# Optimization experiments

Hardware: AMD Instinct MI355X
Metric: run time of the kernel (lower is better)

## Reference

```python
import jax, jax.numpy as jnp
import numpy as np

N_NODES = 100000
N_EDGES = 1600000
HIDDEN_DIM = 64
EIGS_DIM = 32


def setup_inputs() -> dict:
    key = jax.random.key(0)
    k1, k2, k3, k4, k5 = jax.random.split(key, 5)
    q = jax.random.normal(k1, (N_NODES, HIDDEN_DIM), dtype=jnp.float32)
    k = jax.random.normal(k2, (N_NODES, HIDDEN_DIM), dtype=jnp.float32)
    v = jax.random.normal(k3, (N_NODES, HIDDEN_DIM), dtype=jnp.float32)
    eigs = jax.random.normal(k4, (N_NODES, EIGS_DIM), dtype=jnp.float32)
    lambda0 = jnp.zeros((1,), dtype=jnp.float32)  # nn.Parameter(torch.zeros(1))
    indices = jax.random.randint(k5, (2, N_EDGES), 0, N_NODES, dtype=jnp.int64)
    return {"q": q, "k": k, "v": v, "eigs": eigs, "lambda0": lambda0,
            "indices": indices}


def reference(q, k, v, eigs, lambda0, indices):
    n = q.shape[0]
    inv_sqrt_dim = 1.0 / jnp.sqrt(jnp.asarray(q.shape[1], dtype=q.dtype))
    i0 = indices[0]  # destination/row node per edge
    i1 = indices[1]  # source/col node per edge

    # per-edge attention logits: gather-dot-product
    x = jnp.sum(q[i0] * k[i1], axis=-1) * inv_sqrt_dim          # [E]
    y = jnp.sum(eigs[i0] * eigs[i1], axis=-1)                   # [E]
    s = x + jnp.exp(lambda0[0]) * y                             # [E]

    # sparse softmax: clamp(exp(s), -5, 5) then segment-normalize by row sum
    e = jnp.clip(jnp.exp(s), -5.0, 5.0)                         # [E]
    denom = jax.ops.segment_sum(e, i0, num_segments=n)          # [N]
    denom = jnp.where(denom == 0.0, 1.0, denom)
    w = e / denom[i0]                                           # [E]

    # spmm: out[r] = sum_{edges with row r} w_e * v[col_e]
    out = jax.ops.segment_sum(w[:, None] * v[i1], i0, num_segments=n)  # [N, D]
    return out
```

## Files before the change

kernel.cpp:

```cpp
#include <hip/hip_runtime.h>
#include <hip/hip_fp16.h>


#define HD 64
#define ED 32
#define CAP 64
#define RPP 256
#define PSHIFT 8
#define D1 15
#define SLICE 16
#define SPILL_CAP 65536

struct h4 { __half2 a, b; };

__global__ void p1_bin_kernel(const int* __restrict__ idx, int n_edges,
                              int NP, int chunk, int nb, long long pcap,
                              int* __restrict__ part,
                              long long* __restrict__ spill,
                              int* __restrict__ spill_cnt,
                              int* __restrict__ flag,
                              const float* __restrict__ kf,
                              const float* __restrict__ vf,
                              const float* __restrict__ ef,
                              __half* __restrict__ k16,
                              __half* __restrict__ v16,
                              __half* __restrict__ e16,
                              long long nk4, long long ne4) {
    extern __shared__ int sm[];
    int* cnt  = sm;
    int* bins = sm + NP;
    int tid = threadIdx.x;

    for (int i = tid; i < NP; i += 256) cnt[i] = 0;
    __syncthreads();

    int e0 = blockIdx.x * chunk;
    int n  = n_edges - e0; if (n > chunk) n = chunk; if (n < 0) n = 0;

    for (int i = tid; i < n; i += 256) {
        int e = e0 + i;
        int r = idx[e];
        int c = idx[n_edges + e];
        int p = r >> PSHIFT;
        int w = ((r & (RPP - 1)) << 17) | c;
        int pos = atomicAdd(&cnt[p], 1);
        if (pos < D1) {
            bins[p * D1 + pos] = w;
        } else {
            int s = atomicAdd(spill_cnt, 1);
            if (s < SPILL_CAP) spill[s] = ((long long)r << 32) | (unsigned)c;
            else *flag = 1;
        }
    }
    __syncthreads();

    int g16 = tid >> 4;
    int sl  = tid & 15;
    for (int p = g16; p < NP; p += 16) {
        int m = cnt[p]; if (m > D1) m = D1;
        long long base = (long long)p * pcap + (long long)blockIdx.x * SLICE;
        int val = (sl == 0) ? m
                : (sl <= m) ? bins[p * D1 + sl - 1] : 0;
        part[base + sl] = val;
    }

    if (k16 != nullptr) {
        long long gt = (long long)blockIdx.x * 256 + tid;
        long long gs = (long long)gridDim.x * 256;
        for (long long t = gt; t < nk4; t += gs) {
            float4 f = ((const float4*)kf)[t];
            h4 h;
            h.a = __floats2half2_rn(f.x, f.y);
            h.b = __floats2half2_rn(f.z, f.w);
            ((h4*)k16)[t] = h;
        }
        for (long long t = gt; t < nk4; t += gs) {
            float4 f = ((const float4*)vf)[t];
            h4 h;
            h.a = __floats2half2_rn(f.x, f.y);
            h.b = __floats2half2_rn(f.z, f.w);
            ((h4*)v16)[t] = h;
        }
        for (long long t = gt; t < ne4; t += gs) {
            float4 f = ((const float4*)ef)[t];
            h4 h;
            h.a = __floats2half2_rn(f.x, f.y);
            h.b = __floats2half2_rn(f.z, f.w);
            ((h4*)e16)[t] = h;
        }
    }
}

__global__ void p2_bucket_kernel(const int* __restrict__ part,
                                 int* __restrict__ count,
                                 int* __restrict__ bucket, int n_nodes,
                                 int nb, long long pcap) {
    __shared__ int cnt2[RPP / 2];
    __shared__ int win[(RPP / 2) * CAP];
    int tid = threadIdx.x;
    if (tid < RPP / 2) cnt2[tid] = 0;
    __syncthreads();

    int p    = blockIdx.x >> 1;
    int half = blockIdx.x & 1;
    int g  = tid >> 4;
    int sl = tid & 15;
    const int* prow = part + (long long)p * pcap;

    for (int b = g; b < nb; b += 16) {
        int val = prow[b * SLICE + sl];
        int m = __shfl(val, 0, 16);
        if (m > D1) m = D1;
        if (sl >= 1 && sl <= m) {
            int rl = val >> 17;
            if ((rl >> 7) == half) {
                int rh = rl & 127;
                int c  = val & 0x1FFFF;
                int pos = atomicAdd(&cnt2[rh], 1);
                if (pos < CAP) win[(rh << 6) + pos] = c;
            }
        }
    }
    __syncthreads();

    int r0 = (p << PSHIFT) + (half << 7);
    int rows = n_nodes - r0;
    if (rows > RPP / 2) rows = RPP / 2;
    if (rows > 0) {
        int nint4 = rows * (CAP / 4);
        int4* dst = (int4*)(bucket + (long long)r0 * CAP);
        const int4* src = (const int4*)win;
        for (int i = tid; i < nint4; i += 256) dst[i] = src[i];
        if (tid < rows) count[r0 + tid] = cnt2[tid];
    }
}

__global__ void spill_or_zero_kernel(const long long* __restrict__ spill,
                                     const int* __restrict__ spill_cnt,
                                     const int* __restrict__ flag,
                                     int* __restrict__ count,
                                     int* __restrict__ bucket, int n_nodes) {
    int stride = gridDim.x * blockDim.x;
    int t0 = blockIdx.x * blockDim.x + threadIdx.x;
    if (*flag) {
        for (int t = t0; t < n_nodes; t += stride) count[t] = 0;
        return;
    }
    int ns = *spill_cnt; if (ns > SPILL_CAP) ns = SPILL_CAP;
    for (int t = t0; t < ns; t += stride) {
        long long wc = spill[t];
        int r = (int)(wc >> 32);
        int c = (int)(wc & 0xFFFFFFFFLL);
        int pos = atomicAdd(&count[r], 1);
        if (pos < CAP) bucket[(long long)r * CAP + pos] = c;
    }
}

__global__ void repair_scatter_kernel(const int* __restrict__ flag,
                                      const int* __restrict__ idx,
                                      int* __restrict__ count,
                                      int* __restrict__ bucket, int n_edges) {
    if (*flag == 0) return;
    int t = blockIdx.x * blockDim.x + threadIdx.x;
    if (t < n_edges) {
        int r = idx[t];
        int c = idx[n_edges + t];
        int p = atomicAdd(&count[r], 1);
        if (p < CAP) bucket[(long long)r * CAP + p] = c;
    }
}

__global__ void bucket_scatter_kernel(const int* __restrict__ idx,
                                      int* __restrict__ count,
                                      int* __restrict__ bucket, int n_edges) {
    int t = blockIdx.x * blockDim.x + threadIdx.x;
    if (t < n_edges) {
        int r = idx[t];
        int c = idx[n_edges + t];
        int p = atomicAdd(&count[r], 1);
        if (p < CAP) bucket[(long long)r * CAP + p] = c;
    }
}

__global__ void row16_kernel(const float* __restrict__ q,
                             const __half* __restrict__ k16,
                             const __half* __restrict__ v16,
                             const float* __restrict__ eigs,
                             const __half* __restrict__ e16,
                             const float* __restrict__ lambda0,
                             const int* __restrict__ counts,
                             const int* __restrict__ col,
                             const float* __restrict__ kf,
                             const float* __restrict__ vf,
                             const int* __restrict__ idx, int n_edges,
                             float* __restrict__ out, int n_nodes) {
    long long tid = (long long)blockIdx.x * blockDim.x + threadIdx.x;
    int r = (int)(tid >> 6);
    if (r >= n_nodes) return;
    int lane = threadIdx.x & 63;
    int sub = lane & 15;
    int grp = lane >> 4;

    int deg = counts[r];
    const float expL = __expf(lambda0[0]);

    if (deg > CAP) {
        float qs = q[(long long)r * HD + lane] * 0.125f;
        float gs = (lane < ED) ? eigs[(long long)r * ED + lane] * expL : 0.f;
        float accs = 0.f, den = 0.f;
        for (int base = 0; base < n_edges; base += 64) {
            int e = base + lane;
            int rr = (e < n_edges) ? idx[e] : -1;
            int cc = (e < n_edges) ? idx[n_edges + e] : 0;
            unsigned long long mm = __ballot(rr == r);
            while (mm) {
                int b = __ffsll(mm) - 1;
                mm &= mm - 1;
                int c = __shfl(cc, b, 64);
                float kb = kf[(long long)c * HD + lane];
                float gb = (lane < ED) ? eigs[(long long)c * ED + lane] : 0.f;
                float s = qs * kb + gs * gb;
                #pragma unroll
                for (int off = 32; off > 0; off >>= 1) s += __shfl_xor(s, off, 64);
                float e1 = fminf(__expf(s), 5.0f);
                den += e1;
                accs += e1 * vf[(long long)c * HD + lane];
            }
        }
        float inv = (den == 0.f) ? 1.f : __frcp_rn(den);
        out[(long long)r * HD + lane] = accs * inv;
        return;
    }

    long long start = (long long)r * CAP;

    float4 qa = *(const float4*)(q    + (long long)r * HD + sub * 4);
    float2 ga = *(const float2*)(eigs + (long long)r * ED + sub * 2);
    qa.x *= 0.125f; qa.y *= 0.125f; qa.z *= 0.125f; qa.w *= 0.125f;
    ga.x *= expL;   ga.y *= expL;

    float4 acc = make_float4(0.f, 0.f, 0.f, 0.f);
    float den = 0.f;

    for (int base = 0; base < deg; base += 64) {
        int m = deg - base; if (m > 64) m = 64;
        int cl = (lane < m) ? col[start + base + lane] : 0;
        for (int j = 0; j < m; j += 16) {
            int c1 = __shfl(cl, j + grp,      64);
            int c2 = __shfl(cl, j + 4 + grp,  64);
            int c3 = __shfl(cl, j + 8 + grp,  64);
            int c4 = __shfl(cl, j + 12 + grp, 64);
            h4 kb1 = *(const h4*)(k16 + (long long)c1 * HD + sub * 4);
            __half2 gh1 = *(const __half2*)(e16 + (long long)c1 * ED + sub * 2);
            h4 vv1 = *(const h4*)(v16 + (long long)c1 * HD + sub * 4);
            h4 kb2 = *(const h4*)(k16 + (long long)c2 * HD + sub * 4);
            __half2 gh2 = *(const __half2*)(e16 + (long long)c2 * ED + sub * 2);
            h4 vv2 = *(const h4*)(v16 + (long long)c2 * HD + sub * 4);
            h4 kb3 = *(const h4*)(k16 + (long long)c3 * HD + sub * 4);
            __half2 gh3 = *(const __half2*)(e16 + (long long)c3 * ED + sub * 2);
            h4 vv3 = *(const h4*)(v16 + (long long)c3 * HD + sub * 4);
            h4 kb4 = *(const h4*)(k16 + (long long)c4 * HD + sub * 4);
            __half2 gh4 = *(const __half2*)(e16 + (long long)c4 * ED + sub * 2);
            h4 vv4 = *(const h4*)(v16 + (long long)c4 * HD + sub * 4);

            float s1 = qa.x*__low2float(kb1.a) + qa.y*__high2float(kb1.a)
                     + qa.z*__low2float(kb1.b) + qa.w*__high2float(kb1.b)
                     + ga.x*__low2float(gh1)   + ga.y*__high2float(gh1);
            float s2 = qa.x*__low2float(kb2.a) + qa.y*__high2float(kb2.a)
                     + qa.z*__low2float(kb2.b) + qa.w*__high2float(kb2.b)
                     + ga.x*__low2float(gh2)   + ga.y*__high2float(gh2);
            float s3 = qa.x*__low2float(kb3.a) + qa.y*__high2float(kb3.a)
                     + qa.z*__low2float(kb3.b) + qa.w*__high2float(kb3.b)
                     + ga.x*__low2float(gh3)   + ga.y*__high2float(gh3);
            float s4 = qa.x*__low2float(kb4.a) + qa.y*__high2float(kb4.a)
                     + qa.z*__low2float(kb4.b) + qa.w*__high2float(kb4.b)
                     + ga.x*__low2float(gh4)   + ga.y*__high2float(gh4);
            #pragma unroll
            for (int off = 8; off > 0; off >>= 1) {
                s1 += __shfl_xor(s1, off, 64);
                s2 += __shfl_xor(s2, off, 64);
                s3 += __shfl_xor(s3, off, 64);
                s4 += __shfl_xor(s4, off, 64);
            }
            float e1 = fminf(__expf(s1), 5.0f);
            float e2 = fminf(__expf(s2), 5.0f);
            float e3 = fminf(__expf(s3), 5.0f);
            float e4 = fminf(__expf(s4), 5.0f);

            if (j + grp < m) {
                den += e1;
                acc.x += e1 * __low2float(vv1.a); acc.y += e1 * __high2float(vv1.a);
                acc.z += e1 * __low2float(vv1.b); acc.w += e1 * __high2float(vv1.b);
            }
            if (j + 4 + grp < m) {
                den += e2;
                acc.x += e2 * __low2float(vv2.a); acc.y += e2 * __high2float(vv2.a);
                acc.z += e2 * __low2float(vv2.b); acc.w += e2 * __high2float(vv2.b);
            }
            if (j + 8 + grp < m) {
                den += e3;
                acc.x += e3 * __low2float(vv3.a); acc.y += e3 * __high2float(vv3.a);
                acc.z += e3 * __low2float(vv3.b); acc.w += e3 * __high2float(vv3.b);
            }
            if (j + 12 + grp < m) {
                den += e4;
                acc.x += e4 * __low2float(vv4.a); acc.y += e4 * __high2float(vv4.a);
                acc.z += e4 * __low2float(vv4.b); acc.w += e4 * __high2float(vv4.b);
            }
        }
    }

    #pragma unroll
    for (int off = 16; off < 64; off <<= 1) {
        acc.x += __shfl_xor(acc.x, off, 64);
        acc.y += __shfl_xor(acc.y, off, 64);
        acc.z += __shfl_xor(acc.z, off, 64);
        acc.w += __shfl_xor(acc.w, off, 64);
        den   += __shfl_xor(den,   off, 64);
    }

    if (grp == 0) {
        float inv = (den == 0.0f) ? 1.0f : __frcp_rn(den);
        float4 o = make_float4(acc.x * inv, acc.y * inv, acc.z * inv, acc.w * inv);
        *(float4*)(out + (long long)r * HD + sub * 4) = o;
    }
}

__global__ void row_kernel(const float* __restrict__ q, const float* __restrict__ k,
                           const float* __restrict__ v, const float* __restrict__ eigs,
                           const float* __restrict__ lambda0,
                           const int* __restrict__ counts,
                           const int* __restrict__ col,
                           const int* __restrict__ idx, int n_edges,
                           float* __restrict__ out, int n_nodes) {
    long long tid = (long long)blockIdx.x * blockDim.x + threadIdx.x;
    int r = (int)(tid >> 6);
    if (r >= n_nodes) return;
    int lane = threadIdx.x & 63;
    int sub = lane & 15;
    int grp = lane >> 4;

    int deg = counts[r];
    const float expL = __expf(lambda0[0]);

    if (deg > CAP) {
        float qs = q[(long long)r * HD + lane] * 0.125f;
        float gs = (lane < ED) ? eigs[(long long)r * ED + lane] * expL : 0.f;
        float accs = 0.f, den = 0.f;
        for (int base = 0; base < n_edges; base += 64) {
            int e = base + lane;
            int rr = (e < n_edges) ? idx[e] : -1;
            int cc = (e < n_edges) ? idx[n_edges + e] : 0;
            unsigned long long mm = __ballot(rr == r);
            while (mm) {
                int b = __ffsll(mm) - 1;
                mm &= mm - 1;
                int c = __shfl(cc, b, 64);
                float kb = k[(long long)c * HD + lane];
                float gb = (lane < ED) ? eigs[(long long)c * ED + lane] : 0.f;
                float s = qs * kb + gs * gb;
                #pragma unroll
                for (int off = 32; off > 0; off >>= 1) s += __shfl_xor(s, off, 64);
                float e1 = fminf(__expf(s), 5.0f);
                den += e1;
                accs += e1 * v[(long long)c * HD + lane];
            }
        }
        float inv = (den == 0.f) ? 1.f : __frcp_rn(den);
        out[(long long)r * HD + lane] = accs * inv;
        return;
    }

    long long start = (long long)r * CAP;

    float4 qa = *(const float4*)(q    + (long long)r * HD + sub * 4);
    float2 ga = *(const float2*)(eigs + (long long)r * ED + sub * 2);
    qa.x *= 0.125f; qa.y *= 0.125f; qa.z *= 0.125f; qa.w *= 0.125f;
    ga.x *= expL;   ga.y *= expL;

    float4 acc = make_float4(0.f, 0.f, 0.f, 0.f);
    float den = 0.f;

    for (int base = 0; base < deg; base += 64) {
        int m = deg - base; if (m > 64) m = 64;
        int cl = (lane < m) ? col[start + base + lane] : 0;
        for (int j = 0; j < m; j += 8) {
            int c1 = __shfl(cl, j + grp,     64);
            int c2 = __shfl(cl, j + 4 + grp, 64);
            float4 kb1 = *(const float4*)(k    + (long long)c1 * HD + sub * 4);
            float2 gb1 = *(const float2*)(eigs + (long long)c1 * ED + sub * 2);
            float4 vv1 = *(const float4*)(v    + (long long)c1 * HD + sub * 4);
            float4 kb2 = *(const float4*)(k    + (long long)c2 * HD + sub * 4);
            float2 gb2 = *(const float2*)(eigs + (long long)c2 * ED + sub * 2);
            float4 vv2 = *(const float4*)(v    + (long long)c2 * HD + sub * 4);

            float s1 = qa.x*kb1.x + qa.y*kb1.y + qa.z*kb1.z + qa.w*kb1.w
                     + ga.x*gb1.x + ga.y*gb1.y;
            float s2 = qa.x*kb2.x + qa.y*kb2.y + qa.z*kb2.z + qa.w*kb2.w
                     + ga.x*gb2.x + ga.y*gb2.y;
            #pragma unroll
            for (int off = 8; off > 0; off >>= 1) {
                s1 += __shfl_xor(s1, off, 64);
                s2 += __shfl_xor(s2, off, 64);
            }
            float e1 = fminf(__expf(s1), 5.0f);
            float e2 = fminf(__expf(s2), 5.0f);

            if (j + grp < m) {
                den += e1;
                acc.x += e1 * vv1.x; acc.y += e1 * vv1.y;
                acc.z += e1 * vv1.z; acc.w += e1 * vv1.w;
            }
            if (j + 4 + grp < m) {
                den += e2;
                acc.x += e2 * vv2.x; acc.y += e2 * vv2.y;
                acc.z += e2 * vv2.z; acc.w += e2 * vv2.w;
            }
        }
    }

    #pragma unroll
    for (int off = 16; off < 64; off <<= 1) {
        acc.x += __shfl_xor(acc.x, off, 64);
        acc.y += __shfl_xor(acc.y, off, 64);
        acc.z += __shfl_xor(acc.z, off, 64);
        acc.w += __shfl_xor(acc.w, off, 64);
        den   += __shfl_xor(den,   off, 64);
    }

    if (grp == 0) {
        float inv = (den == 0.0f) ? 1.0f : __frcp_rn(den);
        float4 o = make_float4(acc.x * inv, acc.y * inv, acc.z * inv, acc.w * inv);
        *(float4*)(out + (long long)r * HD + sub * 4) = o;
    }
}

__global__ void edge_fused_kernel(const float* __restrict__ q,
                                  const float* __restrict__ k,
                                  const float* __restrict__ v,
                                  const float* __restrict__ eigs,
                                  const float* __restrict__ lambda0,
                                  const int* __restrict__ idx,
                                  float* __restrict__ denom,
                                  float* __restrict__ out, int n_edges) {
    long long gid = (long long)blockIdx.x * blockDim.x + threadIdx.x;
    int lane = threadIdx.x & 63;
    int edge = (int)(gid >> 4);
    int sub  = (int)(gid & 15);
    int valid = (edge < n_edges);
    int ec = valid ? edge : (n_edges - 1);
    int i0 = idx[ec];
    int i1 = idx[n_edges + ec];
    const float expL = __expf(lambda0[0]);
    float4 qa = *(const float4*)(q + (long long)i0 * HD + sub * 4);
    float4 kb = *(const float4*)(k + (long long)i1 * HD + sub * 4);
    float c = (qa.x*kb.x + qa.y*kb.y + qa.z*kb.z + qa.w*kb.w) * 0.125f;
    float2 ea = *(const float2*)(eigs + (long long)i0 * ED + sub * 2);
    float2 eb = *(const float2*)(eigs + (long long)i1 * ED + sub * 2);
    c += expL * (ea.x * eb.x + ea.y * eb.y);
    #pragma unroll
    for (int off = 8; off > 0; off >>= 1) c += __shfl_xor(c, off, 64);
    float e = fminf(__expf(c), 5.0f);
    if (valid && sub == 0) atomicAdd(&denom[i0], e);
    #pragma unroll
    for (int j = 0; j < 4; ++j) {
        float ej = __shfl(e,     j * 16, 64);
        int   r  = __shfl(i0,    j * 16, 64);
        int   s  = __shfl(i1,    j * 16, 64);
        int   vj = __shfl(valid, j * 16, 64);
        if (vj) {
            float vv = v[(long long)s * HD + lane];
            atomicAdd(&out[(long long)r * HD + lane], ej * vv);
        }
    }
}

__global__ void normalize_kernel(float* __restrict__ out,
                                 const float* __restrict__ denom, int n_nodes) {
    int t = blockIdx.x * blockDim.x + threadIdx.x;
    int total = n_nodes * (HD / 4);
    if (t >= total) return;
    int row = t >> 4;
    float d = denom[row];
    float inv = (d == 0.0f) ? 1.0f : __frcp_rn(d);
    float4* o4 = (float4*)out;
    float4 x = o4[t];
    x.x *= inv; x.y *= inv; x.z *= inv; x.w *= inv;
    o4[t] = x;
}

extern "C" void kernel_launch(void* const* d_in, const int* in_sizes, int n_in,
                              void* d_out, int out_size, void* d_ws, size_t ws_size,
                              hipStream_t stream) {
    const float* q       = (const float*)d_in[0];
    const float* k       = (const float*)d_in[1];
    const float* v       = (const float*)d_in[2];
    const float* eigs    = (const float*)d_in[3];
    const float* lambda0 = (const float*)d_in[4];
    const int*   idx     = (const int*)d_in[5];

    const int n_edges = in_sizes[5] / 2;
    const int n_nodes = in_sizes[0] / HD;

    const int NP = (n_nodes + RPP - 1) / RPP;
    const int eb = (n_edges + 255) / 256;
    long long rthreads = (long long)n_nodes * 64;
    const int rb = (int)((rthreads + 255) / 256);

    size_t smbytes = (size_t)NP * (1 + D1) * sizeof(int);
    bool geom_ok = (smbytes <= 60 * 1024) && (n_nodes <= 0x1FFFF);

    size_t fixed = (size_t)n_nodes * sizeof(int)
                 + (size_t)n_nodes * CAP * sizeof(int);
    size_t sp = 8 + (size_t)SPILL_CAP * sizeof(long long);
    size_t h16 = (size_t)n_nodes * (HD + HD + ED) * sizeof(__half);

    auto part_bytes = [&](int nb) {
        return (size_t)NP * (size_t)nb * SLICE * sizeof(int);
    };
    size_t n16_1024 = h16 + fixed + part_bytes(1024) + sp;
    size_t n16_512  = h16 + fixed + part_bytes(512)  + sp;
    size_t n32_1024 = fixed + part_bytes(1024) + sp;
    size_t n32_512  = fixed + part_bytes(512)  + sp;
    size_t need2    = fixed;

    bool use16 = false;
    int nb = 0;
    if (geom_ok && ws_size >= n16_1024)      { use16 = true;  nb = 1024; }
    else if (geom_ok && ws_size >= n16_512)  { use16 = true;  nb = 512;  }
    else if (geom_ok && ws_size >= n32_1024) { use16 = false; nb = 1024; }
    else if (geom_ok && ws_size >= n32_512)  { use16 = false; nb = 512;  }

    if (nb > 0) {
        char* base = (char*)d_ws;
        __half* k16 = nullptr; __half* v16 = nullptr; __half* e16 = nullptr;
        char* ip = base;
        if (use16) {
            k16 = (__half*)base;
            v16 = k16 + (size_t)n_nodes * HD;
            e16 = v16 + (size_t)n_nodes * HD;
            ip = (char*)(e16 + (size_t)n_nodes * ED);
        }
        int* count  = (int*)ip;
        int* bucket = count + n_nodes;
        int* part   = bucket + (size_t)n_nodes * CAP;
        long long pcap = (long long)nb * SLICE;
        int* spill_cnt = part + (size_t)NP * pcap;
        int* flag      = spill_cnt + 1;
        size_t soff = (size_t)((char*)(flag + 1) - base);
        soff = (soff + 7) & ~(size_t)7;
        long long* spill = (long long*)(base + soff);

        hipMemsetAsync(spill_cnt, 0, 2 * sizeof(int), stream);

        int chunk = (n_edges + nb - 1) / nb;
        p1_bin_kernel<<<nb, 256, smbytes, stream>>>(
            idx, n_edges, NP, chunk, nb, pcap, part, spill, spill_cnt, flag,
            k, v, eigs, k16, v16, e16,
            use16 ? (long long)n_nodes * HD / 4 : 0,
            use16 ? (long long)n_nodes * ED / 4 : 0);
        p2_bucket_kernel<<<2 * NP, 256, 0, stream>>>(part, count, bucket,
                                                     n_nodes, nb, pcap);
        spill_or_zero_kernel<<<(n_nodes + 255) / 256, 256, 0, stream>>>(
            spill, spill_cnt, flag, count, bucket, n_nodes);
        repair_scatter_kernel<<<eb, 256, 0, stream>>>(flag, idx, count, bucket,
                                                      n_edges);
        if (use16) {
            row16_kernel<<<rb, 256, 0, stream>>>(q, k16, v16, eigs, e16, lambda0,
                                                 count, bucket, k, v, idx,
                                                 n_edges, (float*)d_out, n_nodes);
        } else {
            row_kernel<<<rb, 256, 0, stream>>>(q, k, v, eigs, lambda0, count,
                                               bucket, idx, n_edges,
                                               (float*)d_out, n_nodes);
        }
    } else if (ws_size >= need2) {
        int* count  = (int*)d_ws;
        int* bucket = count + n_nodes;
        hipMemsetAsync(count, 0, (size_t)n_nodes * sizeof(int), stream);
        bucket_scatter_kernel<<<eb, 256, 0, stream>>>(idx, count, bucket, n_edges);
        row_kernel<<<rb, 256, 0, stream>>>(q, k, v, eigs, lambda0, count, bucket,
                                           idx, n_edges, (float*)d_out, n_nodes);
    } else {
        float* denom = (float*)d_ws;
        hipMemsetAsync(denom, 0, (size_t)n_nodes * sizeof(float), stream);
        hipMemsetAsync(d_out, 0, (size_t)out_size * sizeof(float), stream);
        long long threads = (long long)n_edges * 16;
        int grid = (int)((threads + 255) / 256);
        edge_fused_kernel<<<grid, 256, 0, stream>>>(q, k, v, eigs, lambda0, idx,
                                                    denom, (float*)d_out, n_edges);
        int n4 = n_nodes * (HD / 4);
        normalize_kernel<<<(n4 + 255) / 256, 256, 0, stream>>>((float*)d_out,
                                                               denom, n_nodes);
    }
}
```

Baseline: 259.4 us.

## Fuse bucket construction, spill handling and row attention into one kernel

Replaces the separate bucket-build, spill-or-zero, repair-scatter and row16 kernels with one p2row kernel. Each block assembles its 128-row adjacency window in shared memory, merges spilled edges, or falls back to scanning all edges when the overflow flag is set. It then computes the softmax-weighted aggregation for those rows straight from the shared window. This removes the global count/bucket round trip and three kernel launches. In exchange each block now runs a long serial compute loop with one wave per row over 32 rows, and every block scans the whole spill list.

```diff
diff --git a/kernel.cpp b/kernel.cpp
--- a/kernel.cpp
+++ b/kernel.cpp
@@ -91,10 +91,19 @@
     }
 }
 
-__global__ void p2_bucket_kernel(const int* __restrict__ part,
-                                 int* __restrict__ count,
-                                 int* __restrict__ bucket, int n_nodes,
-                                 int nb, long long pcap) {
+__global__ void p2row_kernel(const int* __restrict__ part,
+                             const long long* __restrict__ spill,
+                             const int* __restrict__ spill_cnt,
+                             const int* __restrict__ flag,
+                             const float* __restrict__ q,
+                             const __half* __restrict__ k16,
+                             const __half* __restrict__ v16,
+                             const float* __restrict__ eigs,
+                             const __half* __restrict__ e16,
+                             const float* __restrict__ lambda0,
+                             const int* __restrict__ idx, int n_edges,
+                             float* __restrict__ out, int n_nodes,
+                             int nb, long long pcap) {
     __shared__ int cnt2[RPP / 2];
     __shared__ int win[(RPP / 2) * CAP];
     int tid = threadIdx.x;
@@ -103,153 +112,105 @@
 
     int p    = blockIdx.x >> 1;
     int half = blockIdx.x & 1;
-    int g  = tid >> 4;
-    int sl = tid & 15;
-    const int* prow = part + (long long)p * pcap;
-
-    for (int b = g; b < nb; b += 16) {
-        int val = prow[b * SLICE + sl];
-        int m = __shfl(val, 0, 16);
-        if (m > D1) m = D1;
-        if (sl >= 1 && sl <= m) {
-            int rl = val >> 17;
-            if ((rl >> 7) == half) {
-                int rh = rl & 127;
-                int c  = val & 0x1FFFF;
+    int r0   = (p << PSHIFT) + (half << 7);
+
+    if (*flag == 0) {
+        int g  = tid >> 4;
+        int sl = tid & 15;
+        const int* prow = part + (long long)p * pcap;
+        for (int b = g; b < nb; b += 16) {
+            int val = prow[b * SLICE + sl];
+            int m = __shfl(val, 0, 16);
+            if (m > D1) m = D1;
+            if (sl >= 1 && sl <= m) {
+                int rl = val >> 17;
+                if ((rl >> 7) == half) {
+                    int rh = rl & 127;
+                    int c  = val & 0x1FFFF;
+                    int pos = atomicAdd(&cnt2[rh], 1);
+                    if (pos < CAP) win[(rh << 6) + pos] = c;
+                }
+            }
+        }
+        int ns = *spill_cnt; if (ns > SPILL_CAP) ns = SPILL_CAP;
+        for (int i = tid; i < ns; i += 256) {
+            long long wc = spill[i];
+            int r = (int)(wc >> 32);
+            if ((r >> PSHIFT) == p && (((r >> 7) & 1) == half)) {
+                int rh = r & 127;
+                int c  = (int)(wc & 0xFFFFFFFFLL);
                 int pos = atomicAdd(&cnt2[rh], 1);
                 if (pos < CAP) win[(rh << 6) + pos] = c;
             }
         }
+    } else {
+        for (int i = tid; i < n_edges; i += 256) {
+            int r = idx[i];
+            if ((r >> PSHIFT) == p && (((r >> 7) & 1) == half)) {
+                int rh = r & 127;
+                int c  = idx[n_edges + i];
+                int pos = atomicAdd(&cnt2[rh], 1);
+                if (pos < CAP) win[(rh << 6) + pos] = c;
+            }
+        }
     }
     __syncthreads();
 
-    int r0 = (p << PSHIFT) + (half << 7);
-    int rows = n_nodes - r0;
-    if (rows > RPP / 2) rows = RPP / 2;
-    if (rows > 0) {
-        int nint4 = rows * (CAP / 4);
-        int4* dst = (int4*)(bucket + (long long)r0 * CAP);
-        const int4* src = (const int4*)win;
-        for (int i = tid; i < nint4; i += 256) dst[i] = src[i];
-        if (tid < rows) count[r0 + tid] = cnt2[tid];
-    }
-}
-
-__global__ void spill_or_zero_kernel(const long long* __restrict__ spill,
-                                     const int* __restrict__ spill_cnt,
-                                     const int* __restrict__ flag,
-                                     int* __restrict__ count,
-                                     int* __restrict__ bucket, int n_nodes) {
-    int stride = gridDim.x * blockDim.x;
-    int t0 = blockIdx.x * blockDim.x + threadIdx.x;
-    if (*flag) {
-        for (int t = t0; t < n_nodes; t += stride) count[t] = 0;
-        return;
-    }
-    int ns = *spill_cnt; if (ns > SPILL_CAP) ns = SPILL_CAP;
-    for (int t = t0; t < ns; t += stride) {
-        long long wc = spill[t];
-        int r = (int)(wc >> 32);
-        int c = (int)(wc & 0xFFFFFFFFLL);
-        int pos = atomicAdd(&count[r], 1);
-        if (pos < CAP) bucket[(long long)r * CAP + pos] = c;
-    }
-}
-
-__global__ void repair_scatter_kernel(const int* __restrict__ flag,
-                                      const int* __restrict__ idx,
-                                      int* __restrict__ count,
-                                      int* __restrict__ bucket, int n_edges) {
-    if (*flag == 0) return;
-    int t = blockIdx.x * blockDim.x + threadIdx.x;
-    if (t < n_edges) {
-        int r = idx[t];
-        int c = idx[n_edges + t];
-        int p = atomicAdd(&count[r], 1);
-        if (p < CAP) bucket[(long long)r * CAP + p] = c;
-    }
-}
-
-__global__ void bucket_scatter_kernel(const int* __restrict__ idx,
-                                      int* __restrict__ count,
-                                      int* __restrict__ bucket, int n_edges) {
-    int t = blockIdx.x * blockDim.x + threadIdx.x;
-    if (t < n_edges) {
-        int r = idx[t];
-        int c = idx[n_edges + t];
-        int p = atomicAdd(&count[r], 1);
-        if (p < CAP) bucket[(long long)r * CAP + p] = c;
-    }
-}
-
-__global__ void row16_kernel(const float* __restrict__ q,
-                             const __half* __restrict__ k16,
-                             const __half* __restrict__ v16,
-                             const float* __restrict__ eigs,
-                             const __half* __restrict__ e16,
-                             const float* __restrict__ lambda0,
-                             const int* __restrict__ counts,
-                             const int* __restrict__ col,
-                             const float* __restrict__ kf,
-                             const float* __restrict__ vf,
-                             const int* __restrict__ idx, int n_edges,
-                             float* __restrict__ out, int n_nodes) {
-    long long tid = (long long)blockIdx.x * blockDim.x + threadIdx.x;
-    int r = (int)(tid >> 6);
-    if (r >= n_nodes) return;
-    int lane = threadIdx.x & 63;
-    int sub = lane & 15;
-    int grp = lane >> 4;
-
-    int deg = counts[r];
+    int wave = tid >> 6;
+    int lane = tid & 63;
+    int sub  = lane & 15;
+    int grp  = lane >> 4;
     const float expL = __expf(lambda0[0]);
 
-    if (deg > CAP) {
-        float qs = q[(long long)r * HD + lane] * 0.125f;
-        float gs = (lane < ED) ? eigs[(long long)r * ED + lane] * expL : 0.f;
-        float accs = 0.f, den = 0.f;
-        for (int base = 0; base < n_edges; base += 64) {
-            int e = base + lane;
-            int rr = (e < n_edges) ? idx[e] : -1;
-            int cc = (e < n_edges) ? idx[n_edges + e] : 0;
-            unsigned long long mm = __ballot(rr == r);
-            while (mm) {
-                int b = __ffsll(mm) - 1;
-                mm &= mm - 1;
-                int c = __shfl(cc, b, 64);
-                float kb = kf[(long long)c * HD + lane];
-                float gb = (lane < ED) ? eigs[(long long)c * ED + lane] : 0.f;
-                float s = qs * kb + gs * gb;
-                #pragma unroll
-                for (int off = 32; off > 0; off >>= 1) s += __shfl_xor(s, off, 64);
-                float e1 = fminf(__expf(s), 5.0f);
-                den += e1;
-                accs += e1 * vf[(long long)c * HD + lane];
-            }
-        }
-        float inv = (den == 0.f) ? 1.f : __frcp_rn(den);
-        out[(long long)r * HD + lane] = accs * inv;
-        return;
-    }
-
-    long long start = (long long)r * CAP;
-
-    float4 qa = *(const float4*)(q    + (long long)r * HD + sub * 4);
-    float2 ga = *(const float2*)(eigs + (long long)r * ED + sub * 2);
-    qa.x *= 0.125f; qa.y *= 0.125f; qa.z *= 0.125f; qa.w *= 0.125f;
-    ga.x *= expL;   ga.y *= expL;
-
-    float4 acc = make_float4(0.f, 0.f, 0.f, 0.f);
-    float den = 0.f;
-
-    for (int base = 0; base < deg; base += 64) {
-        int m = deg - base; if (m > 64) m = 64;
-        int cl = (lane < m) ? col[start + base + lane] : 0;
-        for (int j = 0; j < m; j += 16) {
-            int c1 = __shfl(cl, j + grp,      64);
-            int c2 = __shfl(cl, j + 4 + grp,  64);
-            int c3 = __shfl(cl, j + 8 + grp,  64);
-            int c4 = __shfl(cl, j + 12 + grp, 64);
+    for (int rw = wave; rw < RPP / 2; rw += 4) {
+        int r = r0 + rw;
+        if (r >= n_nodes) continue;
+        int deg = cnt2[rw];
+
+        if (deg > CAP) {
+            float qs = q[(long long)r * HD + lane] * 0.125f;
+            float gs = (lane < ED) ? eigs[(long long)r * ED + lane] * expL : 0.f;
+            float accs = 0.f, den = 0.f;
+            for (int base = 0; base < n_edges; base += 64) {
+                int e = base + lane;
+                int rr = (e < n_edges) ? idx[e] : -1;
+                int cc = (e < n_edges) ? idx[n_edges + e] : 0;
+                unsigned long long mm = __ballot(rr == r);
+                while (mm) {
+                    int b = __ffsll(mm) - 1;
+                    mm &= mm - 1;
+                    int c = __shfl(cc, b, 64);
+                    float kb = __half2float(k16[(long long)c * HD + lane]);
+                    float gb = (lane < ED)
+                             ? __half2float(e16[(long long)c * ED + lane]) : 0.f;
+                    float s = qs * kb + gs * gb;
+                    #pragma unroll
+                    for (int off = 32; off > 0; off >>= 1)
+                        s += __shfl_xor(s, off, 64);
+                    float e1 = fminf(__expf(s), 5.0f);
+                    den += e1;
+                    accs += e1 * __half2float(v16[(long long)c * HD + lane]);
+                }
+            }
+            float inv = (den == 0.f) ? 1.f : __frcp_rn(den);
+            out[(long long)r * HD + lane] = accs * inv;
+            continue;
+        }
+
+        float4 qa = *(const float4*)(q    + (long long)r * HD + sub * 4);
+        float2 ga = *(const float2*)(eigs + (long long)r * ED + sub * 2);
+        qa.x *= 0.125f; qa.y *= 0.125f; qa.z *= 0.125f; qa.w *= 0.125f;
+        ga.x *= expL;   ga.y *= expL;
+
+        float4 acc = make_float4(0.f, 0.f, 0.f, 0.f);
+        float den = 0.f;
+        const int* cl = &win[rw << 6];
+
+        for (int j = 0; j < deg; j += 16) {
+            int c1 = (j + grp      < deg) ? cl[j + grp]      : 0;
+            int c2 = (j + 4 + grp  < deg) ? cl[j + 4 + grp]  : 0;
+            int c3 = (j + 8 + grp  < deg) ? cl[j + 8 + grp]  : 0;
+            int c4 = (j + 12 + grp < deg) ? cl[j + 12 + grp] : 0;
             h4 kb1 = *(const h4*)(k16 + (long long)c1 * HD + sub * 4);
             __half2 gh1 = *(const __half2*)(e16 + (long long)c1 * ED + sub * 2);
             h4 vv1 = *(const h4*)(v16 + (long long)c1 * HD + sub * 4);
@@ -287,42 +248,135 @@
             float e3 = fminf(__expf(s3), 5.0f);
             float e4 = fminf(__expf(s4), 5.0f);
 
-            if (j + grp < m) {
+            if (j + grp < deg) {
                 den += e1;
                 acc.x += e1 * __low2float(vv1.a); acc.y += e1 * __high2float(vv1.a);
                 acc.z += e1 * __low2float(vv1.b); acc.w += e1 * __high2float(vv1.b);
             }
-            if (j + 4 + grp < m) {
+            if (j + 4 + grp < deg) {
                 den += e2;
                 acc.x += e2 * __low2float(vv2.a); acc.y += e2 * __high2float(vv2.a);
                 acc.z += e2 * __low2float(vv2.b); acc.w += e2 * __high2float(vv2.b);
             }
-            if (j + 8 + grp < m) {
+            if (j + 8 + grp < deg) {
                 den += e3;
                 acc.x += e3 * __low2float(vv3.a); acc.y += e3 * __high2float(vv3.a);
                 acc.z += e3 * __low2float(vv3.b); acc.w += e3 * __high2float(vv3.b);
             }
-            if (j + 12 + grp < m) {
+            if (j + 12 + grp < deg) {
                 den += e4;
                 acc.x += e4 * __low2float(vv4.a); acc.y += e4 * __high2float(vv4.a);
                 acc.z += e4 * __low2float(vv4.b); acc.w += e4 * __high2float(vv4.b);
             }
         }
-    }
-
-    #pragma unroll
-    for (int off = 16; off < 64; off <<= 1) {
-        acc.x += __shfl_xor(acc.x, off, 64);
-        acc.y += __shfl_xor(acc.y, off, 64);
-        acc.z += __shfl_xor(acc.z, off, 64);
-        acc.w += __shfl_xor(acc.w, off, 64);
-        den   += __shfl_xor(den,   off, 64);
-    }
-
-    if (grp == 0) {
-        float inv = (den == 0.0f) ? 1.0f : __frcp_rn(den);
-        float4 o = make_float4(acc.x * inv, acc.y * inv, acc.z * inv, acc.w * inv);
-        *(float4*)(out + (long long)r * HD + sub * 4) = o;
+
+        #pragma unroll
+        for (int off = 16; off < 64; off <<= 1) {
+            acc.x += __shfl_xor(acc.x, off, 64);
+            acc.y += __shfl_xor(acc.y, off, 64);
+            acc.z += __shfl_xor(acc.z, off, 64);
+            acc.w += __shfl_xor(acc.w, off, 64);
+            den   += __shfl_xor(den,   off, 64);
+        }
+
+        if (grp == 0) {
+            float inv = (den == 0.0f) ? 1.0f : __frcp_rn(den);
+            float4 o = make_float4(acc.x * inv, acc.y * inv,
+                                   acc.z * inv, acc.w * inv);
+            *(float4*)(out + (long long)r * HD + sub * 4) = o;
+        }
+    }
+}
+
+
+__global__ void p2_bucket_kernel(const int* __restrict__ part,
+                                 int* __restrict__ count,
+                                 int* __restrict__ bucket, int n_nodes,
+                                 int nb, long long pcap) {
+    __shared__ int cnt2[RPP / 2];
+    __shared__ int win[(RPP / 2) * CAP];
+    int tid = threadIdx.x;
+    if (tid < RPP / 2) cnt2[tid] = 0;
+    __syncthreads();
+
+    int p    = blockIdx.x >> 1;
+    int half = blockIdx.x & 1;
+    int g  = tid >> 4;
+    int sl = tid & 15;
+    const int* prow = part + (long long)p * pcap;
+
+    for (int b = g; b < nb; b += 16) {
+        int val = prow[b * SLICE + sl];
+        int m = __shfl(val, 0, 16);
+        if (m > D1) m = D1;
+        if (sl >= 1 && sl <= m) {
+            int rl = val >> 17;
+            if ((rl >> 7) == half) {
+                int rh = rl & 127;
+                int c  = val & 0x1FFFF;
+                int pos = atomicAdd(&cnt2[rh], 1);
+                if (pos < CAP) win[(rh << 6) + pos] = c;
+            }
+        }
+    }
+    __syncthreads();
+
+    int r0 = (p << PSHIFT) + (half << 7);
+    int rows = n_nodes - r0;
+    if (rows > RPP / 2) rows = RPP / 2;
+    if (rows > 0) {
+        int nint4 = rows * (CAP / 4);
+        int4* dst = (int4*)(bucket + (long long)r0 * CAP);
+        const int4* src = (const int4*)win;
+        for (int i = tid; i < nint4; i += 256) dst[i] = src[i];
+        if (tid < rows) count[r0 + tid] = cnt2[tid];
+    }
+}
+
+__global__ void spill_or_zero_kernel(const long long* __restrict__ spill,
+                                     const int* __restrict__ spill_cnt,
+                                     const int* __restrict__ flag,
+                                     int* __restrict__ count,
+                                     int* __restrict__ bucket, int n_nodes) {
+    int stride = gridDim.x * blockDim.x;
+    int t0 = blockIdx.x * blockDim.x + threadIdx.x;
+    if (*flag) {
+        for (int t = t0; t < n_nodes; t += stride) count[t] = 0;
+        return;
+    }
+    int ns = *spill_cnt; if (ns > SPILL_CAP) ns = SPILL_CAP;
+    for (int t = t0; t < ns; t += stride) {
+        long long wc = spill[t];
+        int r = (int)(wc >> 32);
+        int c = (int)(wc & 0xFFFFFFFFLL);
+        int pos = atomicAdd(&count[r], 1);
+        if (pos < CAP) bucket[(long long)r * CAP + pos] = c;
+    }
+}
+
+__global__ void repair_scatter_kernel(const int* __restrict__ flag,
+                                      const int* __restrict__ idx,
+                                      int* __restrict__ count,
+                                      int* __restrict__ bucket, int n_edges) {
+    if (*flag == 0) return;
+    int t = blockIdx.x * blockDim.x + threadIdx.x;
+    if (t < n_edges) {
+        int r = idx[t];
+        int c = idx[n_edges + t];
+        int p = atomicAdd(&count[r], 1);
+        if (p < CAP) bucket[(long long)r * CAP + p] = c;
+    }
+}
+
+__global__ void bucket_scatter_kernel(const int* __restrict__ idx,
+                                      int* __restrict__ count,
+                                      int* __restrict__ bucket, int n_edges) {
+    int t = blockIdx.x * blockDim.x + threadIdx.x;
+    if (t < n_edges) {
+        int r = idx[t];
+        int c = idx[n_edges + t];
+        int p = atomicAdd(&count[r], 1);
+        if (p < CAP) bucket[(long long)r * CAP + p] = c;
     }
 }
 
@@ -510,41 +564,29 @@
     size_t smbytes = (size_t)NP * (1 + D1) * sizeof(int);
     bool geom_ok = (smbytes <= 60 * 1024) && (n_nodes <= 0x1FFFF);
 
+    size_t sp  = 8 + (size_t)SPILL_CAP * sizeof(long long);
+    size_t h16 = (size_t)n_nodes * (HD + HD + ED) * sizeof(__half);
     size_t fixed = (size_t)n_nodes * sizeof(int)
                  + (size_t)n_nodes * CAP * sizeof(int);
-    size_t sp = 8 + (size_t)SPILL_CAP * sizeof(long long);
-    size_t h16 = (size_t)n_nodes * (HD + HD + ED) * sizeof(__half);
-
     auto part_bytes = [&](int nb) {
         return (size_t)NP * (size_t)nb * SLICE * sizeof(int);
     };
-    size_t n16_1024 = h16 + fixed + part_bytes(1024) + sp;
-    size_t n16_512  = h16 + fixed + part_bytes(512)  + sp;
+    size_t n16_1024 = h16 + part_bytes(1024) + sp;
+    size_t n16_512  = h16 + part_bytes(512)  + sp;
     size_t n32_1024 = fixed + part_bytes(1024) + sp;
-    size_t n32_512  = fixed + part_bytes(512)  + sp;
     size_t need2    = fixed;
 
-    bool use16 = false;
-    int nb = 0;
-    if (geom_ok && ws_size >= n16_1024)      { use16 = true;  nb = 1024; }
-    else if (geom_ok && ws_size >= n16_512)  { use16 = true;  nb = 512;  }
-    else if (geom_ok && ws_size >= n32_1024) { use16 = false; nb = 1024; }
-    else if (geom_ok && ws_size >= n32_512)  { use16 = false; nb = 512;  }
-
-    if (nb > 0) {
+    int nb16 = 0;
+    if (geom_ok && ws_size >= n16_1024)      nb16 = 1024;
+    else if (geom_ok && ws_size >= n16_512)  nb16 = 512;
+
+    if (nb16 > 0) {
         char* base = (char*)d_ws;
-        __half* k16 = nullptr; __half* v16 = nullptr; __half* e16 = nullptr;
-        char* ip = base;
-        if (use16) {
-            k16 = (__half*)base;
-            v16 = k16 + (size_t)n_nodes * HD;
-            e16 = v16 + (size_t)n_nodes * HD;
-            ip = (char*)(e16 + (size_t)n_nodes * ED);
-        }
-        int* count  = (int*)ip;
-        int* bucket = count + n_nodes;
-        int* part   = bucket + (size_t)n_nodes * CAP;
-        long long pcap = (long long)nb * SLICE;
+        __half* k16 = (__half*)base;
+        __half* v16 = k16 + (size_t)n_nodes * HD;
+        __half* e16 = v16 + (size_t)n_nodes * HD;
+        int* part = (int*)(e16 + (size_t)n_nodes * ED);
+        long long pcap = (long long)nb16 * SLICE;
         int* spill_cnt = part + (size_t)NP * pcap;
         int* flag      = spill_cnt + 1;
         size_t soff = (size_t)((char*)(flag + 1) - base);
@@ -553,27 +595,40 @@
 
         hipMemsetAsync(spill_cnt, 0, 2 * sizeof(int), stream);
 
-        int chunk = (n_edges + nb - 1) / nb;
-        p1_bin_kernel<<<nb, 256, smbytes, stream>>>(
-            idx, n_edges, NP, chunk, nb, pcap, part, spill, spill_cnt, flag,
+        int chunk = (n_edges + nb16 - 1) / nb16;
+        p1_bin_kernel<<<nb16, 256, smbytes, stream>>>(
+            idx, n_edges, NP, chunk, nb16, pcap, part, spill, spill_cnt, flag,
             k, v, eigs, k16, v16, e16,
-            use16 ? (long long)n_nodes * HD / 4 : 0,
-            use16 ? (long long)n_nodes * ED / 4 : 0);
+            (long long)n_nodes * HD / 4, (long long)n_nodes * ED / 4);
+        p2row_kernel<<<2 * NP, 256, 0, stream>>>(
+            part, spill, spill_cnt, flag, q, k16, v16, eigs, e16, lambda0,
+            idx, n_edges, (float*)d_out, n_nodes, nb16, pcap);
+    } else if (geom_ok && ws_size >= n32_1024) {
+        char* base = (char*)d_ws;
+        int* count  = (int*)base;
+        int* bucket = count + n_nodes;
+        int* part   = bucket + (size_t)n_nodes * CAP;
+        long long pcap = (long long)1024 * SLICE;
+        int* spill_cnt = part + (size_t)NP * pcap;
+        int* flag      = spill_cnt + 1;
+        size_t soff = (size_t)((char*)(flag + 1) - base);
+        soff = (soff + 7) & ~(size_t)7;
+        long long* spill = (long long*)(base + soff);
+
+        hipMemsetAsync(spill_cnt, 0, 2 * sizeof(int), stream);
+
+        int chunk = (n_edges + 1023) / 1024;
+        p1_bin_kernel<<<1024, 256, smbytes, stream>>>(
+            idx, n_edges, NP, chunk, 1024, pcap, part, spill, spill_cnt, flag,
+            nullptr, nullptr, nullptr, nullptr, nullptr, nullptr, 0, 0);
         p2_bucket_kernel<<<2 * NP, 256, 0, stream>>>(part, count, bucket,
-                                                     n_nodes, nb, pcap);
+                                                     n_nodes, 1024, pcap);
         spill_or_zero_kernel<<<(n_nodes + 255) / 256, 256, 0, stream>>>(
             spill, spill_cnt, flag, count, bucket, n_nodes);
         repair_scatter_kernel<<<eb, 256, 0, stream>>>(flag, idx, count, bucket,
                                                       n_edges);
-        if (use16) {
-            row16_kernel<<<rb, 256, 0, stream>>>(q, k16, v16, eigs, e16, lambda0,
-                                                 count, bucket, k, v, idx,
-                                                 n_edges, (float*)d_out, n_nodes);
-        } else {
-            row_kernel<<<rb, 256, 0, stream>>>(q, k, v, eigs, lambda0, count,
-                                               bucket, idx, n_edges,
-                                               (float*)d_out, n_nodes);
-        }
+        row_kernel<<<rb, 256, 0, stream>>>(q, k, v, eigs, lambda0, count, bucket,
+                                           idx, n_edges, (float*)d_out, n_nodes);
     } else if (ws_size >= need2) {
         int* count  = (int*)d_ws;
         int* bucket = count + n_nodes;
```

Result: slower. 281.7 us (+8.6%).

## Split bin and fp16-convert blocks, fold spill and repair into bucket kernel

Applied to the files above, without the earlier changes.

The binning kernel now launches twice as many blocks. The first half bins edges into partitions and the second half converts k, v and eigs to fp16, so the two tasks run on separate blocks instead of serially inside each block. The spill-merge and flag-repair kernels are removed. Their work moves into p2_bucket_kernel, which scans the spill list (or the full edge list on overflow) and keeps only the entries for its own row range, saving two kernel launches. The partition count is fixed at 512 bins, and each p2 block now re-reads the whole spill list, so that redundant read grows if the spill list is large.

```diff
diff --git a/kernel.cpp b/kernel.cpp
--- a/kernel.cpp
+++ b/kernel.cpp
@@ -9,27 +9,57 @@
 #define PSHIFT 8
 #define D1 15
 #define SLICE 16
+#define NBIN 512
 #define SPILL_CAP 65536
 
 struct h4 { __half2 a, b; };
 
-__global__ void p1_bin_kernel(const int* __restrict__ idx, int n_edges,
-                              int NP, int chunk, int nb, long long pcap,
-                              int* __restrict__ part,
-                              long long* __restrict__ spill,
-                              int* __restrict__ spill_cnt,
-                              int* __restrict__ flag,
-                              const float* __restrict__ kf,
-                              const float* __restrict__ vf,
-                              const float* __restrict__ ef,
-                              __half* __restrict__ k16,
-                              __half* __restrict__ v16,
-                              __half* __restrict__ e16,
-                              long long nk4, long long ne4) {
+__global__ void p1_wide_kernel(const int* __restrict__ idx, int n_edges,
+                               int NP, int chunk, long long pcap,
+                               int* __restrict__ part,
+                               long long* __restrict__ spill,
+                               int* __restrict__ spill_cnt,
+                               int* __restrict__ flag,
+                               const float* __restrict__ kf,
+                               const float* __restrict__ vf,
+                               const float* __restrict__ ef,
+                               __half* __restrict__ k16,
+                               __half* __restrict__ v16,
+                               __half* __restrict__ e16,
+                               long long nk4, long long ne4) {
     extern __shared__ int sm[];
+    int tid = threadIdx.x;
+
+    if (blockIdx.x >= NBIN) {
+        if (k16 == nullptr) return;
+        long long gt = (long long)(blockIdx.x - NBIN) * 256 + tid;
+        long long gs = (long long)(gridDim.x - NBIN) * 256;
+        for (long long t = gt; t < nk4; t += gs) {
+            float4 f = ((const float4*)kf)[t];
+            h4 h;
+            h.a = __floats2half2_rn(f.x, f.y);
+            h.b = __floats2half2_rn(f.z, f.w);
+            ((h4*)k16)[t] = h;
+        }
+        for (long long t = gt; t < nk4; t += gs) {
+            float4 f = ((const float4*)vf)[t];
+            h4 h;
+            h.a = __floats2half2_rn(f.x, f.y);
+            h.b = __floats2half2_rn(f.z, f.w);
+            ((h4*)v16)[t] = h;
+        }
+        for (long long t = gt; t < ne4; t += gs) {
+            float4 f = ((const float4*)ef)[t];
+            h4 h;
+            h.a = __floats2half2_rn(f.x, f.y);
+            h.b = __floats2half2_rn(f.z, f.w);
+            ((h4*)e16)[t] = h;
+        }
+        return;
+    }
+
     int* cnt  = sm;
     int* bins = sm + NP;
-    int tid = threadIdx.x;
 
     for (int i = tid; i < NP; i += 256) cnt[i] = 0;
     __syncthreads();
@@ -63,38 +93,16 @@
                 : (sl <= m) ? bins[p * D1 + sl - 1] : 0;
         part[base + sl] = val;
     }
-
-    if (k16 != nullptr) {
-        long long gt = (long long)blockIdx.x * 256 + tid;
-        long long gs = (long long)gridDim.x * 256;
-        for (long long t = gt; t < nk4; t += gs) {
-            float4 f = ((const float4*)kf)[t];
-            h4 h;
-            h.a = __floats2half2_rn(f.x, f.y);
-            h.b = __floats2half2_rn(f.z, f.w);
-            ((h4*)k16)[t] = h;
-        }
-        for (long long t = gt; t < nk4; t += gs) {
-            float4 f = ((const float4*)vf)[t];
-            h4 h;
-            h.a = __floats2half2_rn(f.x, f.y);
-            h.b = __floats2half2_rn(f.z, f.w);
-            ((h4*)v16)[t] = h;
-        }
-        for (long long t = gt; t < ne4; t += gs) {
-            float4 f = ((const float4*)ef)[t];
-            h4 h;
-            h.a = __floats2half2_rn(f.x, f.y);
-            h.b = __floats2half2_rn(f.z, f.w);
-            ((h4*)e16)[t] = h;
-        }
-    }
 }
 
 __global__ void p2_bucket_kernel(const int* __restrict__ part,
+                                 const long long* __restrict__ spill,
+                                 const int* __restrict__ spill_cnt,
+                                 const int* __restrict__ flag,
+                                 const int* __restrict__ idx, int n_edges,
                                  int* __restrict__ count,
                                  int* __restrict__ bucket, int n_nodes,
-                                 int nb, long long pcap) {
+                                 long long pcap) {
     __shared__ int cnt2[RPP / 2];
     __shared__ int win[(RPP / 2) * CAP];
     int tid = threadIdx.x;
@@ -103,19 +111,42 @@
 
     int p    = blockIdx.x >> 1;
     int half = blockIdx.x & 1;
-    int g  = tid >> 4;
-    int sl = tid & 15;
-    const int* prow = part + (long long)p * pcap;
-
-    for (int b = g; b < nb; b += 16) {
-        int val = prow[b * SLICE + sl];
-        int m = __shfl(val, 0, 16);
-        if (m > D1) m = D1;
-        if (sl >= 1 && sl <= m) {
-            int rl = val >> 17;
-            if ((rl >> 7) == half) {
-                int rh = rl & 127;
-                int c  = val & 0x1FFFF;
+
+    if (*flag == 0) {
+        int g  = tid >> 4;
+        int sl = tid & 15;
+        const int* prow = part + (long long)p * pcap;
+        for (int b = g; b < NBIN; b += 16) {
+            int val = prow[b * SLICE + sl];
+            int m = __shfl(val, 0, 16);
+            if (m > D1) m = D1;
+            if (sl >= 1 && sl <= m) {
+                int rl = val >> 17;
+                if ((rl >> 7) == half) {
+                    int rh = rl & 127;
+                    int c  = val & 0x1FFFF;
+                    int pos = atomicAdd(&cnt2[rh], 1);
+                    if (pos < CAP) win[(rh << 6) + pos] = c;
+                }
+            }
+        }
+        int ns = *spill_cnt; if (ns > SPILL_CAP) ns = SPILL_CAP;
+        for (int i = tid; i < ns; i += 256) {
+            long long wc = spill[i];
+            int r = (int)(wc >> 32);
+            if ((r >> PSHIFT) == p && (((r >> 7) & 1) == half)) {
+                int rh = r & 127;
+                int c  = (int)(wc & 0xFFFFFFFFLL);
+                int pos = atomicAdd(&cnt2[rh], 1);
+                if (pos < CAP) win[(rh << 6) + pos] = c;
+            }
+        }
+    } else {
+        for (int i = tid; i < n_edges; i += 256) {
+            int r = idx[i];
+            if ((r >> PSHIFT) == p && (((r >> 7) & 1) == half)) {
+                int rh = r & 127;
+                int c  = idx[n_edges + i];
                 int pos = atomicAdd(&cnt2[rh], 1);
                 if (pos < CAP) win[(rh << 6) + pos] = c;
             }
@@ -132,41 +163,6 @@
         const int4* src = (const int4*)win;
         for (int i = tid; i < nint4; i += 256) dst[i] = src[i];
         if (tid < rows) count[r0 + tid] = cnt2[tid];
-    }
-}
-
-__global__ void spill_or_zero_kernel(const long long* __restrict__ spill,
-                                     const int* __restrict__ spill_cnt,
-                                     const int* __restrict__ flag,
-                                     int* __restrict__ count,
-                                     int* __restrict__ bucket, int n_nodes) {
-    int stride = gridDim.x * blockDim.x;
-    int t0 = blockIdx.x * blockDim.x + threadIdx.x;
-    if (*flag) {
-        for (int t = t0; t < n_nodes; t += stride) count[t] = 0;
-        return;
-    }
-    int ns = *spill_cnt; if (ns > SPILL_CAP) ns = SPILL_CAP;
-    for (int t = t0; t < ns; t += stride) {
-        long long wc = spill[t];
-        int r = (int)(wc >> 32);
-        int c = (int)(wc & 0xFFFFFFFFLL);
-        int pos = atomicAdd(&count[r], 1);
-        if (pos < CAP) bucket[(long long)r * CAP + pos] = c;
-    }
-}
-
-__global__ void repair_scatter_kernel(const int* __restrict__ flag,
-                                      const int* __restrict__ idx,
-                                      int* __restrict__ count,
-                                      int* __restrict__ bucket, int n_edges) {
-    if (*flag == 0) return;
-    int t = blockIdx.x * blockDim.x + threadIdx.x;
-    if (t < n_edges) {
-        int r = idx[t];
-        int c = idx[n_edges + t];
-        int p = atomicAdd(&count[r], 1);
-        if (p < CAP) bucket[(long long)r * CAP + p] = c;
     }
 }
 
@@ -510,41 +506,26 @@
     size_t smbytes = (size_t)NP * (1 + D1) * sizeof(int);
     bool geom_ok = (smbytes <= 60 * 1024) && (n_nodes <= 0x1FFFF);
 
+    size_t sp  = 8 + (size_t)SPILL_CAP * sizeof(long long);
+    size_t h16 = (size_t)n_nodes * (HD + HD + ED) * sizeof(__half);
     size_t fixed = (size_t)n_nodes * sizeof(int)
                  + (size_t)n_nodes * CAP * sizeof(int);
-    size_t sp = 8 + (size_t)SPILL_CAP * sizeof(long long);
-    size_t h16 = (size_t)n_nodes * (HD + HD + ED) * sizeof(__half);
-
-    auto part_bytes = [&](int nb) {
-        return (size_t)NP * (size_t)nb * SLICE * sizeof(int);
-    };
-    size_t n16_1024 = h16 + fixed + part_bytes(1024) + sp;
-    size_t n16_512  = h16 + fixed + part_bytes(512)  + sp;
-    size_t n32_1024 = fixed + part_bytes(1024) + sp;
-    size_t n32_512  = fixed + part_bytes(512)  + sp;
-    size_t need2    = fixed;
-
-    bool use16 = false;
-    int nb = 0;
-    if (geom_ok && ws_size >= n16_1024)      { use16 = true;  nb = 1024; }
-    else if (geom_ok && ws_size >= n16_512)  { use16 = true;  nb = 512;  }
-    else if (geom_ok && ws_size >= n32_1024) { use16 = false; nb = 1024; }
-    else if (geom_ok && ws_size >= n32_512)  { use16 = false; nb = 512;  }
-
-    if (nb > 0) {
+    size_t pbytes = (size_t)NP * (size_t)NBIN * SLICE * sizeof(int);
+    size_t n16 = h16 + fixed + pbytes + sp;
+    size_t n32 = fixed + pbytes + sp;
+    size_t need2 = fixed;
+
+    long long pcap = (long long)NBIN * SLICE;
+    int chunk = (n_edges + NBIN - 1) / NBIN;
+
+    if (geom_ok && ws_size >= n16) {
         char* base = (char*)d_ws;
-        __half* k16 = nullptr; __half* v16 = nullptr; __half* e16 = nullptr;
-        char* ip = base;
-        if (use16) {
-            k16 = (__half*)base;
-            v16 = k16 + (size_t)n_nodes * HD;
-            e16 = v16 + (size_t)n_nodes * HD;
-            ip = (char*)(e16 + (size_t)n_nodes * ED);
-        }
-        int* count  = (int*)ip;
+        __half* k16 = (__half*)base;
+        __half* v16 = k16 + (size_t)n_nodes * HD;
+        __half* e16 = v16 + (size_t)n_nodes * HD;
+        int* count  = (int*)(e16 + (size_t)n_nodes * ED);
         int* bucket = count + n_nodes;
         int* part   = bucket + (size_t)n_nodes * CAP;
-        long long pcap = (long long)nb * SLICE;
         int* spill_cnt = part + (size_t)NP * pcap;
         int* flag      = spill_cnt + 1;
         size_t soff = (size_t)((char*)(flag + 1) - base);
@@ -553,27 +534,37 @@
 
         hipMemsetAsync(spill_cnt, 0, 2 * sizeof(int), stream);
 
-        int chunk = (n_edges + nb - 1) / nb;
-        p1_bin_kernel<<<nb, 256, smbytes, stream>>>(
-            idx, n_edges, NP, chunk, nb, pcap, part, spill, spill_cnt, flag,
+        p1_wide_kernel<<<2 * NBIN, 256, smbytes, stream>>>(
+            idx, n_edges, NP, chunk, pcap, part, spill, spill_cnt, flag,
             k, v, eigs, k16, v16, e16,
-            use16 ? (long long)n_nodes * HD / 4 : 0,
-            use16 ? (long long)n_nodes * ED / 4 : 0);
-        p2_bucket_kernel<<<2 * NP, 256, 0, stream>>>(part, count, bucket,
-                                                     n_nodes, nb, pcap);
-        spill_or_zero_kernel<<<(n_nodes + 255) / 256, 256, 0, stream>>>(
-            spill, spill_cnt, flag, count, bucket, n_nodes);
-        repair_scatter_kernel<<<eb, 256, 0, stream>>>(flag, idx, count, bucket,
-                                                      n_edges);
-        if (use16) {
-            row16_kernel<<<rb, 256, 0, stream>>>(q, k16, v16, eigs, e16, lambda0,
-                                                 count, bucket, k, v, idx,
-                                                 n_edges, (float*)d_out, n_nodes);
-        } else {
-            row_kernel<<<rb, 256, 0, stream>>>(q, k, v, eigs, lambda0, count,
-                                               bucket, idx, n_edges,
-                                               (float*)d_out, n_nodes);
-        }
+            (long long)n_nodes * HD / 4, (long long)n_nodes * ED / 4);
+        p2_bucket_kernel<<<2 * NP, 256, 0, stream>>>(
+            part, spill, spill_cnt, flag, idx, n_edges, count, bucket,
+            n_nodes, pcap);
+        row16_kernel<<<rb, 256, 0, stream>>>(q, k16, v16, eigs, e16, lambda0,
+                                             count, bucket, k, v, idx, n_edges,
+                                             (float*)d_out, n_nodes);
+    } else if (geom_ok && ws_size >= n32) {
+        char* base = (char*)d_ws;
+        int* count  = (int*)base;
+        int* bucket = count + n_nodes;
+        int* part   = bucket + (size_t)n_nodes * CAP;
+        int* spill_cnt = part + (size_t)NP * pcap;
+        int* flag      = spill_cnt + 1;
+        size_t soff = (size_t)((char*)(flag + 1) - base);
+        soff = (soff + 7) & ~(size_t)7;
+        long long* spill = (long long*)(base + soff);
+
+        hipMemsetAsync(spill_cnt, 0, 2 * sizeof(int), stream);
+
+        p1_wide_kernel<<<2 * NBIN, 256, smbytes, stream>>>(
+            idx, n_edges, NP, chunk, pcap, part, spill, spill_cnt, flag,
+            nullptr, nullptr, nullptr, nullptr, nullptr, nullptr, 0, 0);
+        p2_bucket_kernel<<<2 * NP, 256, 0, stream>>>(
+            part, spill, spill_cnt, flag, idx, n_edges, count, bucket,
+            n_nodes, pcap);
+        row_kernel<<<rb, 256, 0, stream>>>(q, k, v, eigs, lambda0, count, bucket,
+                                           idx, n_edges, (float*)d_out, n_nodes);
     } else if (ws_size >= need2) {
         int* count  = (int*)d_ws;
         int* bucket = count + n_nodes;
```

Measured after the change: 261.1 us. Within noise of the previous version (+0.7%).
